# Optimization experiments

Hardware: AMD Instinct MI355X
Metric: run time of the kernel (lower is better)

The kernel has to match this reference:

```python
import jax, jax.numpy as jnp
import numpy as np
import math

B, S, E, D = 8, 2048, 1024, 1024  # batch, seq, emb_dim, encoder_emb_dim
LN_EPS = 1e-5
CLAMP = 1.0e9

def setup_inputs() -> dict:
    key = jax.random.key(0)
    ks = jax.random.split(key, 6)
    s = 1.0 / math.sqrt(E)
    return {
        "x": jax.random.normal(ks[0], (B, S, E), dtype=jnp.float32),
        "ln_w": jnp.ones((E,), jnp.float32),
        "ln_b": jnp.zeros((E,), jnp.float32),
        "wq": jax.random.normal(ks[1], (E, D), jnp.float32) * s,
        "bq": jnp.zeros((D,), jnp.float32),
        "wk": jax.random.normal(ks[2], (E, D), jnp.float32) * s,
        "bk": jnp.zeros((D,), jnp.float32),
        "wv": jax.random.normal(ks[3], (E, D), jnp.float32) * s,
        "bv": jnp.zeros((D,), jnp.float32),
        "w0": jax.random.normal(ks[4], (D, E), jnp.float32) * (1.0 / math.sqrt(D)),
        "b0": jnp.zeros((E,), jnp.float32),
    }

def reference(x, ln_w, ln_b, wq, bq, wk, bk, wv, bv, w0, b0):
    # LayerNorm over last dim (torch default eps=1e-5)
    mu = jnp.mean(x, axis=-1, keepdims=True)
    var = jnp.mean(jnp.square(x - mu), axis=-1, keepdims=True)
    xn = (x - mu) * jax.lax.rsqrt(var + LN_EPS) * ln_w + ln_b

    q = xn @ wq + bq  # [B,S,D]
    k = xn @ wk + bk
    v = xn @ wv + bv

    scale = math.sqrt(D) + 1e-9
    scores = jnp.einsum("bsd,btd->bst", q, k) / scale
    scores = jnp.clip(scores, -CLAMP, CLAMP)

    # masking=True, self_attending=True: mask = tril(ones, diagonal=-1)
    # i.e. positions t < s get -inf; diagonal stays unmasked (no NaN rows).
    mask = jnp.tril(jnp.ones((S, S), dtype=bool), k=-1)
    scores = jnp.where(mask, -jnp.inf, scores)

    a = jax.nn.softmax(scores, axis=-1)
    h = jnp.einsum("bst,btd->bsd", a, v)
    return h @ w0 + b0
```

## Files before the change

### kernel.cpp

```cpp
#include <hip/hip_runtime.h>
#include <cmath>

using u16 = unsigned short;
using u32 = unsigned int;
using bf16x8 = __attribute__((ext_vector_type(8))) __bf16;
using f32x4  = __attribute__((ext_vector_type(4))) float;

__device__ inline u16 f2bf(float f) {
  u32 u = __float_as_uint(f);
  u32 r = (u + 0x7fffu + ((u >> 16) & 1u)) >> 16;
  return (u16)r;
}

__global__ __launch_bounds__(256) void ln_kernel(
    const float* __restrict__ x, const float* __restrict__ w,
    const float* __restrict__ b, u16* __restrict__ xn) {
  int row = blockIdx.x;
  const float4* xr = (const float4*)(x + (size_t)row * 1024);
  float4 v = xr[threadIdx.x];
  float s  = v.x + v.y + v.z + v.w;
  float ss = v.x * v.x + v.y * v.y + v.z * v.z + v.w * v.w;
  int lane = threadIdx.x & 63, wave = threadIdx.x >> 6;
#pragma unroll
  for (int o = 32; o >= 1; o >>= 1) {
    s  += __shfl_xor(s, o, 64);
    ss += __shfl_xor(ss, o, 64);
  }
  __shared__ float rs[4], rq[4];
  if (lane == 0) { rs[wave] = s; rq[wave] = ss; }
  __syncthreads();
  s  = rs[0] + rs[1] + rs[2] + rs[3];
  ss = rq[0] + rq[1] + rq[2] + rq[3];
  float mean = s * (1.0f / 1024.0f);
  float var  = ss * (1.0f / 1024.0f) - mean * mean;
  float rstd = rsqrtf(var + 1e-5f);
  int c = threadIdx.x * 4;
  ushort4 ov;
  ov.x = f2bf((v.x - mean) * rstd * w[c + 0] + b[c + 0]);
  ov.y = f2bf((v.y - mean) * rstd * w[c + 1] + b[c + 1]);
  ov.z = f2bf((v.z - mean) * rstd * w[c + 2] + b[c + 2]);
  ov.w = f2bf((v.w - mean) * rstd * w[c + 3] + b[c + 3]);
  ((ushort4*)(xn + (size_t)row * 1024))[threadIdx.x] = ov;
}

__global__ __launch_bounds__(256) void transpose_w(
    const float* __restrict__ in, u16* __restrict__ out, int R, int C) {
  __shared__ float tile[32][33];
  int c0 = blockIdx.x * 32, r0 = blockIdx.y * 32;
  int tx = threadIdx.x, ty = threadIdx.y;
#pragma unroll
  for (int i = 0; i < 32; i += 8)
    tile[ty + i][tx] = in[(size_t)(r0 + ty + i) * C + c0 + tx];
  __syncthreads();
#pragma unroll
  for (int i = 0; i < 32; i += 8)
    out[(size_t)(c0 + ty + i) * R + r0 + tx] = f2bf(tile[tx][ty + i]);
}

__global__ void concat_bias(const float* __restrict__ bq, const float* __restrict__ bk,
                            const float* __restrict__ bv, float* __restrict__ o) {
  int i = blockIdx.x * 1024 + threadIdx.x;
  const float* src = (blockIdx.x == 0) ? bq : (blockIdx.x == 1) ? bk : bv;
  o[i] = src[threadIdx.x];
}

__global__ void rowinv_kernel(const float* __restrict__ sumP,
                              float* __restrict__ inv, int bA) {
  int r = blockIdx.x * 256 + threadIdx.x;
  int bz = bA + (r >> 11), s = r & 2047;
  float t = 0.f;
  for (int tj = s >> 8; tj < 8; ++tj)
    t += sumP[((size_t)bz * 8 + tj) * 2048 + s];
  inv[(size_t)bz * 2048 + s] = 1.0f / t;
}

template <int OUTF32, int MODE>
__global__ __launch_bounds__(512, 2) void gemm256(
    const u16* __restrict__ A, const u16* __restrict__ B, void* __restrict__ Cv,
    const float* __restrict__ bias, int K, int lda, int ldb, int ldc,
    float scale, long long sA, long long sB, long long sC) {
  int gx = gridDim.x;
  int wg = blockIdx.y * gx + blockIdx.x;
  {
    int nwg = gx * gridDim.y;
    if ((nwg & 7) == 0) {
      int q = nwg >> 3;
      wg = (wg & 7) * q + (wg >> 3);
    }
  }
  const int ti = wg / gx, tj = wg % gx, bz = blockIdx.z;
  if (MODE == 1 && tj < ti) return;

  const u16* Ab = A + (size_t)bz * (size_t)sA;
  const u16* Bb = B + (size_t)bz * (size_t)sB;

  __shared__ u16 As[2][256 * 64];
  __shared__ u16 Bs[2][256 * 64];

  const int tid = threadIdx.x;
  const int wave = tid >> 6, lane = tid & 63;
  const int wr = wave >> 2, wc = wave & 3;
  const int fr = lane & 15;
  const int kb16 = (lane >> 4) * 16;
  const int swz = (fr & 7) << 4;
  const int cs0 = kb16 ^ swz;
  const int cs1 = (64 + kb16) ^ swz;
  const int aRowOff = (wr * 128 + fr) * 128;
  const int bRowOff = (wc * 64 + fr) * 128;

  size_t gAo[2][2], gBo[2][2];
  u32 ldsA[2][2], ldsB[2][2];
#pragma unroll
  for (int h = 0; h < 2; ++h) {
#pragma unroll
    for (int l = 0; l < 2; ++l) {
      int i = l * 512 + tid;
      int rih = i >> 3, ch8 = i & 7;
      int rA = (rih & 63) + ((rih >> 6) << 7) + h * 64;
      int cbA = (ch8 << 4) ^ ((rA & 7) << 4);
      gAo[h][l] = (size_t)rA * lda + (cbA >> 1);
      ldsA[h][l] = (u32)(rA * 8 + ch8) * 16;
      int rB = (rih & 31) + ((rih >> 5) << 6) + h * 32;
      int cbB = (ch8 << 4) ^ ((rB & 7) << 4);
      gBo[h][l] = (size_t)rB * ldb + (cbB >> 1);
      ldsB[h][l] = (u32)(rB * 8 + ch8) * 16;
    }
  }
  const size_t aBase = (size_t)(ti * 256) * lda;
  const size_t bBase = (size_t)(tj * 256) * ldb;

  const int k0 = (MODE == 2) ? ti * 256 : 0;
  const int niter = (K - k0) / 128;

  f32x4 acc[8][4] = {};
  bf16x8 aF[4][2], bF[4][2];

#define GLL(gaddr, laddr)                                        \
  __builtin_amdgcn_global_load_lds(                              \
      (const __attribute__((address_space(1))) void*)(gaddr),    \
      (__attribute__((address_space(3))) void*)(laddr), 16, 0, 0)

#define STAGE_A(buf, h, t)                                                     \
  do {                                                                         \
    const size_t _kt = aBase + (size_t)(k0 + (t) * 64);                        \
    GLL(Ab + _kt + gAo[h][0], (char*)&As[buf][0] + ldsA[h][0]);                \
    GLL(Ab + _kt + gAo[h][1], (char*)&As[buf][0] + ldsA[h][1]);                \
  } while (0)
#define STAGE_B(buf, h, t)                                                     \
  do {                                                                         \
    const size_t _kt = bBase + (size_t)(k0 + (t) * 64);                        \
    GLL(Bb + _kt + gBo[h][0], (char*)&Bs[buf][0] + ldsB[h][0]);                \
    GLL(Bb + _kt + gBo[h][1], (char*)&Bs[buf][0] + ldsB[h][1]);                \
  } while (0)

#define DS_A(buf, qm)                                                \
  do {                                                               \
    const char* _pa = (const char*)&As[buf][0] + aRowOff + (qm)*8192;\
    _Pragma("unroll") for (int mm = 0; mm < 4; ++mm) {               \
      aF[mm][0] = *(const bf16x8*)(_pa + mm * 2048 + cs0);           \
      aF[mm][1] = *(const bf16x8*)(_pa + mm * 2048 + cs1);           \
    }                                                                \
  } while (0)
#define DS_B(buf, nh)                                                \
  do {                                                               \
    const char* _pb = (const char*)&Bs[buf][0] + bRowOff;            \
    _Pragma("unroll") for (int nn = 0; nn < 2; ++nn) {               \
      bF[(nh)*2 + nn][0] = *(const bf16x8*)(_pb + ((nh)*2 + nn) * 2048 + cs0); \
      bF[(nh)*2 + nn][1] = *(const bf16x8*)(_pb + ((nh)*2 + nn) * 2048 + cs1); \
    }                                                                \
  } while (0)

#define MMA(qm, nh)                                                          \
  do {                                                                       \
    _Pragma("unroll") for (int mm = 0; mm < 4; ++mm)                         \
    _Pragma("unroll") for (int nn = 0; nn < 2; ++nn) {                       \
      f32x4 _c = acc[(qm)*4 + mm][(nh)*2 + nn];                              \
      _c = __builtin_amdgcn_mfma_f32_16x16x32_bf16(aF[mm][0], bF[(nh)*2+nn][0], _c, 0, 0, 0); \
      _c = __builtin_amdgcn_mfma_f32_16x16x32_bf16(aF[mm][1], bF[(nh)*2+nn][1], _c, 0, 0, 0); \
      acc[(qm)*4 + mm][(nh)*2 + nn] = _c;                                    \
    }                                                                        \
  } while (0)

#define BAR __builtin_amdgcn_s_barrier()
#define LGKM0 asm volatile("s_waitcnt lgkmcnt(0)" ::: "memory")
#define VM6 asm volatile("s_waitcnt vmcnt(6)" ::: "memory")
#define VM0 asm volatile("s_waitcnt vmcnt(0)" ::: "memory")
#define PRIO1 __builtin_amdgcn_s_setprio(1)
#define PRIO0 __builtin_amdgcn_s_setprio(0)

  STAGE_B(0, 0, 0); STAGE_B(0, 1, 0); STAGE_A(0, 0, 0); STAGE_A(0, 1, 0);
  STAGE_B(1, 0, 1); STAGE_B(1, 1, 1); STAGE_A(1, 0, 1);
  VM6; BAR;

  for (int it = 0; it < niter; ++it) {
    const bool last = (it == niter - 1);
    const int t1g = 2 * it + 1, t2g = 2 * it + 2, t3g = 2 * it + 3;

    DS_A(0, 0); DS_B(0, 0);
    STAGE_A(1, 1, t1g);
    BAR; LGKM0; PRIO1; MMA(0, 0); PRIO0; BAR;
    DS_B(0, 1);
    if (!last) STAGE_B(0, 0, t2g);
    BAR; LGKM0; PRIO1; MMA(0, 1); PRIO0; BAR;
    DS_A(0, 1);
    if (!last) STAGE_B(0, 1, t2g);
    BAR; LGKM0; PRIO1; MMA(1, 0); PRIO0; BAR;
    if (!last) STAGE_A(0, 0, t2g);
    BAR; PRIO1; MMA(1, 1); PRIO0;
    if (last) { VM0; } else { VM6; }
    BAR;
    DS_A(1, 0); DS_B(1, 0);
    if (!last) STAGE_A(0, 1, t2g);
    BAR; LGKM0; PRIO1; MMA(0, 0); PRIO0; BAR;
    DS_B(1, 1);
    if (!last) STAGE_B(1, 0, t3g);
    BAR; LGKM0; PRIO1; MMA(0, 1); PRIO0; BAR;
    DS_A(1, 1);
    if (!last) STAGE_B(1, 1, t3g);
    BAR; LGKM0; PRIO1; MMA(1, 0); PRIO0; BAR;
    if (!last) STAGE_A(1, 0, t3g);
    BAR; PRIO1; MMA(1, 1); PRIO0;
    if (!last) VM6;
    BAR;
  }

  const int orow0 = ti * 256 + wr * 128 + ((lane >> 4) << 2);
  const int ocol0 = tj * 256 + wc * 64 + fr;
#pragma unroll
  for (int m = 0; m < 8; ++m) {
#pragma unroll
    for (int n = 0; n < 4; ++n) {
      const int col = ocol0 + n * 16;
      const float bv = bias ? bias[col] : 0.0f;
#pragma unroll
      for (int j = 0; j < 4; ++j) {
        const int row = orow0 + m * 16 + j;
        const float v = acc[m][n][j] * scale + bv;
        const size_t idx = (size_t)bz * (size_t)sC + (size_t)row * ldc + col;
        if (OUTF32) ((float*)Cv)[idx] = v;
        else        ((u16*)Cv)[idx]   = f2bf(v);
      }
    }
  }
#undef GLL
#undef STAGE_A
#undef STAGE_B
#undef DS_A
#undef DS_B
#undef MMA
#undef BAR
#undef LGKM0
#undef VM6
#undef VM0
#undef PRIO1
#undef PRIO0
}

template <int BM, int EPI, int LDA, int LDB, int LDC, int KK, int K0CT>
__device__ __forceinline__ void gemm_body(
    const u16* __restrict__ Ab, const u16* __restrict__ Bb,
    void* __restrict__ Cp, const float* __restrict__ bias,
    int rk0, float scale, size_t cbase, int ti, int tj,
    u16* __restrict__ AsP, u16* __restrict__ BsP,
    float* __restrict__ sumP, int diag, const float* __restrict__ invRow) {
  constexpr int WM = BM / 2;
  constexpr int MH = BM / 64;
  constexpr int FM = 2 * MH;
  constexpr int HR = BM / 4;
  constexpr int LA = BM / 128;

  const int k0 = (K0CT >= 0) ? K0CT : rk0;

  const int tid = threadIdx.x;
  const int wave = tid >> 6, lane = tid & 63;
  const int wr = wave >> 2, wc = wave & 3;
  const int fr = lane & 15;
  const int kb16 = (lane >> 4) * 16;
  const int swz = (fr & 7) << 4;
  const int cs0 = kb16 ^ swz;
  const int cs1 = (64 + kb16) ^ swz;
  const int aRowOff = (wr * WM + fr) * 128;
  const int bRowOff = (wc * 64 + fr) * 128;

  size_t gAo[2][LA], gBo[2][2];
  u32 ldsA[2][LA], ldsB[2][2];
#pragma unroll
  for (int h = 0; h < 2; ++h) {
#pragma unroll
    for (int l = 0; l < LA; ++l) {
      int i = l * 512 + tid;
      int rih = i >> 3, ch8 = i & 7;
      int rA = (rih % HR) + (rih / HR) * WM + h * HR;
      int cbA = (ch8 << 4) ^ ((rA & 7) << 4);
      gAo[h][l] = (size_t)rA * LDA + (cbA >> 1);
      ldsA[h][l] = (u32)(rA * 8 + ch8) * 16;
    }
#pragma unroll
    for (int l = 0; l < 2; ++l) {
      int i = l * 512 + tid;
      int rih = i >> 3, ch8 = i & 7;
      int rB = (rih & 31) + ((rih >> 5) << 6) + h * 32;
      int cbB = (ch8 << 4) ^ ((rB & 7) << 4);
      gBo[h][l] = (size_t)rB * LDB + (cbB >> 1);
      ldsB[h][l] = (u32)(rB * 8 + ch8) * 16;
    }
  }
  const size_t aBase = (size_t)(ti * BM) * LDA;
  const size_t bBase = (size_t)(tj * 256) * LDB;
  const int niter = (KK - k0) / 128;

  f32x4 acc[FM][4] = {};
  bf16x8 aF[MH][2], bF[4][2];

#define GLL(gaddr, laddr)                                        \
  __builtin_amdgcn_global_load_lds(                              \
      (const __attribute__((address_space(1))) void*)(gaddr),    \
      (__attribute__((address_space(3))) void*)(laddr), 16, 0, 0)

#define STAGE_A(buf, h, t)                                                   \
  do {                                                                       \
    const size_t _kt = aBase + (size_t)(k0 + (t) * 64);                      \
    _Pragma("unroll") for (int _l = 0; _l < LA; ++_l)                        \
        GLL(Ab + _kt + gAo[h][_l],                                           \
            (char*)(AsP + (buf) * (BM * 64)) + ldsA[h][_l]);                 \
  } while (0)
#define STAGE_B(buf, h, t)                                                   \
  do {                                                                       \
    const size_t _kt = bBase + (size_t)(k0 + (t) * 64);                      \
    _Pragma("unroll") for (int _l = 0; _l < 2; ++_l)                         \
        GLL(Bb + _kt + gBo[h][_l],                                           \
            (char*)(BsP + (buf) * (256 * 64)) + ldsB[h][_l]);                \
  } while (0)

#define DS_A(buf, qm)                                                        \
  do {                                                                       \
    const char* _pa =                                                        \
        (const char*)(AsP + (buf) * (BM * 64)) + aRowOff + (qm) * (MH * 2048); \
    _Pragma("unroll") for (int mm = 0; mm < MH; ++mm) {                      \
      aF[mm][0] = *(const bf16x8*)(_pa + mm * 2048 + cs0);                   \
      aF[mm][1] = *(const bf16x8*)(_pa + mm * 2048 + cs1);                   \
    }                                                                        \
  } while (0)
#define DS_B(buf, nh)                                                        \
  do {                                                                       \
    const char* _pb = (const char*)(BsP + (buf) * (256 * 64)) + bRowOff;     \
    _Pragma("unroll") for (int nn = 0; nn < 2; ++nn) {                       \
      bF[(nh)*2 + nn][0] = *(const bf16x8*)(_pb + ((nh)*2 + nn) * 2048 + cs0); \
      bF[(nh)*2 + nn][1] = *(const bf16x8*)(_pb + ((nh)*2 + nn) * 2048 + cs1); \
    }                                                                        \
  } while (0)

#define MMA(qm, nh)                                                          \
  do {                                                                       \
    _Pragma("unroll") for (int mm = 0; mm < MH; ++mm)                        \
    _Pragma("unroll") for (int nn = 0; nn < 2; ++nn) {                       \
      f32x4 _c = acc[(qm)*MH + mm][(nh)*2 + nn];                             \
      _c = __builtin_amdgcn_mfma_f32_16x16x32_bf16(aF[mm][0], bF[(nh)*2+nn][0], _c, 0, 0, 0); \
      _c = __builtin_amdgcn_mfma_f32_16x16x32_bf16(aF[mm][1], bF[(nh)*2+nn][1], _c, 0, 0, 0); \
      acc[(qm)*MH + mm][(nh)*2 + nn] = _c;                                   \
    }                                                                        \
  } while (0)

#define BAR __builtin_amdgcn_s_barrier()
#define LGKM0 asm volatile("s_waitcnt lgkmcnt(0)" ::: "memory")
#define VMN                                                                  \
  do {                                                                       \
    if constexpr (BM == 256)                                                 \
      asm volatile("s_waitcnt vmcnt(6)" ::: "memory");                       \
    else                                                                     \
      asm volatile("s_waitcnt vmcnt(5)" ::: "memory");                       \
  } while (0)
#define VM0 asm volatile("s_waitcnt vmcnt(0)" ::: "memory")
#define PRIO1 __builtin_amdgcn_s_setprio(1)
#define PRIO0 __builtin_amdgcn_s_setprio(0)

  STAGE_B(0, 0, 0); STAGE_B(0, 1, 0); STAGE_A(0, 0, 0); STAGE_A(0, 1, 0);
  STAGE_B(1, 0, 1); STAGE_B(1, 1, 1); STAGE_A(1, 0, 1);
  VMN; BAR;

#pragma unroll 1
  for (int it = 0; it < niter; ++it) {
    const bool last = (it == niter - 1);
    const int t1g = 2 * it + 1, t2g = 2 * it + 2, t3g = 2 * it + 3;

    DS_A(0, 0); DS_B(0, 0);
    STAGE_A(1, 1, t1g);
    BAR; LGKM0; PRIO1; MMA(0, 0); PRIO0; BAR;
    DS_B(0, 1);
    if (!last) STAGE_B(0, 0, t2g);
    BAR; LGKM0; PRIO1; MMA(0, 1); PRIO0; BAR;
    DS_A(0, 1);
    if (!last) STAGE_B(0, 1, t2g);
    BAR; LGKM0; PRIO1; MMA(1, 0); PRIO0; BAR;
    if (!last) STAGE_A(0, 0, t2g);
    BAR; PRIO1; MMA(1, 1); PRIO0;
    if (last) { VM0; } else { VMN; }
    BAR;
    DS_A(1, 0); DS_B(1, 0);
    if (!last) STAGE_A(0, 1, t2g);
    BAR; LGKM0; PRIO1; MMA(0, 0); PRIO0; BAR;
    DS_B(1, 1);
    if (!last) STAGE_B(1, 0, t3g);
    BAR; LGKM0; PRIO1; MMA(0, 1); PRIO0; BAR;
    DS_A(1, 1);
    if (!last) STAGE_B(1, 1, t3g);
    BAR; LGKM0; PRIO1; MMA(1, 0); PRIO0; BAR;
    if (!last) STAGE_A(1, 0, t3g);
    BAR; PRIO1; MMA(1, 1); PRIO0;
    if (!last) VMN;
    BAR;
  }

  const int orow0 = ti * BM + wr * WM + ((lane >> 4) << 2);
  const int ocol0 = tj * 256 + wc * 64 + fr;

  if constexpr (EPI == 1) {
    float* slds = (float*)AsP;
    const int rl0 = wr * WM + ((lane >> 4) << 2);
#pragma unroll
    for (int m = 0; m < FM; ++m) {
#pragma unroll
      for (int j = 0; j < 4; ++j) {
        const int rl = rl0 + m * 16 + j;
        const int row = ti * BM + rl;
        float rsum = 0.f;
#pragma unroll
        for (int n = 0; n < 4; ++n) {
          const int cl = wc * 64 + fr + n * 16;
          float v = acc[m][n][j] * scale;
          v = fminf(fmaxf(v, -1.0e9f), 1.0e9f);
          v = fminf(v, 60.0f);
          float e = __expf(v - 5.0f);
          if (diag && cl < rl) e = 0.f;
          rsum += e;
          ((u16*)Cp)[cbase + (size_t)row * LDC + ocol0 + n * 16] = f2bf(e);
        }
        rsum += __shfl_xor(rsum, 1, 64);
        rsum += __shfl_xor(rsum, 2, 64);
        rsum += __shfl_xor(rsum, 4, 64);
        rsum += __shfl_xor(rsum, 8, 64);
        if (fr == 0) slds[rl * 4 + wc] = rsum;
      }
    }
    __syncthreads();
    if (tid < 256) {
      float t = slds[tid * 4 + 0] + slds[tid * 4 + 1] +
                slds[tid * 4 + 2] + slds[tid * 4 + 3];
      sumP[ti * BM + tid] = t;
    }
  } else {
#pragma unroll
    for (int m = 0; m < FM; ++m) {
#pragma unroll
      for (int j = 0; j < 4; ++j) {
        const int row = orow0 + m * 16 + j;
        float mul = (EPI == 2) ? invRow[row] : 1.0f;
#pragma unroll
        for (int n = 0; n < 4; ++n) {
          const int col = ocol0 + n * 16;
          const float bv = bias ? bias[col] : 0.0f;
          const size_t idx = cbase + (size_t)row * LDC + col;
          if constexpr (EPI == 2) {
            ((float*)Cp)[idx] = acc[m][n][j] * mul + bv;
          } else {
            ((u16*)Cp)[idx] = f2bf(acc[m][n][j] + bv);
          }
        }
      }
    }
  }
#undef GLL
#undef STAGE_A
#undef STAGE_B
#undef DS_A
#undef DS_B
#undef MMA
#undef BAR
#undef LGKM0
#undef VMN
#undef VM0
#undef PRIO1
#undef PRIO0
}

__global__ __launch_bounds__(512, 2) void gemm_qkwt(
    const u16* __restrict__ QKVp, const u16* __restrict__ w0t,
    u16* __restrict__ Wt, u16* __restrict__ sc, float* __restrict__ sumP,
    int wtBlocks, int b0, int nb, float qk_scale) {
  __shared__ u16 As[2][256 * 64];
  __shared__ u16 Bs[2][256 * 64];
  const long long sQKV = 2048LL * 3072, sWt = 1024LL * 2048, sS = 2048LL * 2048;
  int x = blockIdx.x;
  if (x < wtBlocks) {
    int r = x & 7, o = x >> 3;
    int ti = o & 3, bztj = r + 8 * (o >> 2);
    int bz = bztj >> 3, tj = bztj & 7;
    gemm_body<256, 0, 1024, 3072, 2048, 1024, 0>(
        w0t, QKVp + (size_t)bz * sQKV + 2048, Wt, nullptr, 0, 1.0f,
        (size_t)bz * sWt, ti, tj, &As[0][0], &Bs[0][0], nullptr, 0, nullptr);
  } else {
    int q = x - wtBlocks;
    int bzl = q % nb, t36 = q / nb;
    int bz = b0 + bzl;
    int tj = 0, accm = 0;
    while (t36 >= accm + tj + 1) { accm += tj + 1; ++tj; }
    int tq = t36 - accm;
    const u16* Ab = QKVp + (size_t)bz * sQKV;
    gemm_body<256, 1, 3072, 3072, 2048, 1024, 0>(
        Ab, Ab + 1024, sc, nullptr, 0, qk_scale, (size_t)bzl * sS,
        tq, tj, &As[0][0], &Bs[0][0],
        sumP + ((size_t)bz * 8 + tj) * 2048, tq == tj, nullptr);
  }
}

__global__ __launch_bounds__(512, 2) void gemm_pv(
    const u16* __restrict__ sc, const u16* __restrict__ Wt,
    float* __restrict__ out, const float* __restrict__ b0v,
    const float* __restrict__ inv, int nb, int bA) {
  __shared__ u16 As[2][128 * 64];
  __shared__ u16 Bs[2][256 * 64];
  const long long sP = 2048LL * 2048, sWt = 1024LL * 2048, sH = 2048LL * 1024;
  int x = blockIdx.x;
  int bzl = x % nb;
  int rem = x / nb;
  int ti = rem >> 2, tj = rem & 3;
  int bz = bA + bzl;
  gemm_body<128, 2, 2048, 2048, 1024, 2048, -1>(
      sc + (size_t)bzl * sP, Wt + (size_t)bz * sWt, out, b0v, ti * 128, 1.0f,
      (size_t)bz * sH, ti, tj, &As[0][0], &Bs[0][0], nullptr, 0,
      inv + (size_t)bz * 2048);
}

extern "C" void kernel_launch(void* const* d_in, const int* in_sizes, int n_in,
                              void* d_out, int out_size, void* d_ws, size_t ws_size,
                              hipStream_t stream) {
  (void)in_sizes; (void)n_in; (void)out_size;
  const float* x   = (const float*)d_in[0];
  const float* lnw = (const float*)d_in[1];
  const float* lnb = (const float*)d_in[2];
  const float* wq  = (const float*)d_in[3];
  const float* bq  = (const float*)d_in[4];
  const float* wk  = (const float*)d_in[5];
  const float* bk  = (const float*)d_in[6];
  const float* wv  = (const float*)d_in[7];
  const float* bv  = (const float*)d_in[8];
  const float* w0  = (const float*)d_in[9];
  const float* b0  = (const float*)d_in[10];
  float* out = (float*)d_out;

  const size_t ROWS = 16384;
  char* ws = (char*)d_ws;
  size_t off = 0;
  auto alloc = [&](size_t bytes) -> void* {
    void* p = ws + off;
    off += (bytes + 255) & ~(size_t)255;
    return p;
  };
  u16*   xn    = (u16*)alloc(ROWS * 1024 * 2);
  u16*   wqkvt = (u16*)alloc((size_t)3072 * 1024 * 2);
  u16*   w0t   = (u16*)alloc((size_t)1024 * 1024 * 2);
  float* bqkv  = (float*)alloc(3072 * 4);
  float* sumP  = (float*)alloc((size_t)8 * 8 * 2048 * 4);
  float* inv   = (float*)alloc((size_t)8 * 2048 * 4);
  u16*   QKV   = (u16*)alloc(ROWS * 3072 * 2);
  u16*   Wt    = (u16*)alloc(ROWS * 1024 * 2);

  const size_t CHUNK1 = (size_t)2048 * 2048 * 2;
  size_t avail = (ws_size > off) ? ws_size - off : 0;
  int NBCH = (int)(avail / CHUNK1);
  if (NBCH > 8) NBCH = 8;
  if (NBCH < 1) NBCH = 1;
  u16* sc = (u16*)(ws + off);

  ln_kernel<<<dim3(16384), dim3(256), 0, stream>>>(x, lnw, lnb, xn);
  dim3 tb(32, 8);
  transpose_w<<<dim3(32, 32), tb, 0, stream>>>(wq, wqkvt, 1024, 1024);
  transpose_w<<<dim3(32, 32), tb, 0, stream>>>(wk, wqkvt + (size_t)1024 * 1024, 1024, 1024);
  transpose_w<<<dim3(32, 32), tb, 0, stream>>>(wv, wqkvt + (size_t)2048 * 1024, 1024, 1024);
  transpose_w<<<dim3(32, 32), tb, 0, stream>>>(w0, w0t, 1024, 1024);
  concat_bias<<<dim3(3), dim3(1024), 0, stream>>>(bq, bk, bv, bqkv);

  gemm256<0, 0><<<dim3(12, 64, 1), dim3(512), 0, stream>>>(
      xn, wqkvt, QKV, bqkv, 1024, 1024, 1024, 3072, 1.0f, 0, 0, 0);

  float qk_scale = (float)(1.0 / (std::sqrt(1024.0) + 1e-9));

  for (int bA = 0; bA < 8; bA += NBCH) {
    int nb = 8 - bA;
    if (nb > NBCH) nb = NBCH;
    int wtB = (bA == 0) ? 256 : 0;
    gemm_qkwt<<<dim3(wtB + nb * 36), dim3(512), 0, stream>>>(
        QKV, w0t, Wt, sc, sumP, wtB, bA, nb, qk_scale);
    rowinv_kernel<<<dim3(nb * 8), dim3(256), 0, stream>>>(sumP, inv, bA);
    gemm_pv<<<dim3(64 * nb), dim3(512), 0, stream>>>(
        sc, Wt, out, b0, inv, nb, bA);
  }
}
```

Measured before the change: 325.3 us.

## Fold row-inverse into PV GEMM, merge weight transposes, reorder QK/Wt blocks

The four weight transpose launches become one launch with a z-dimension. The separate rowinv kernel is removed: each PV GEMM workgroup now sums the partial softmax row sums and computes their reciprocals into LDS in its prologue. In the combined QK/Wt kernel, the QK score blocks are now dispatched first, and the Wt (w0ᵀ·V) blocks are split into 128-row tiles, twice as many blocks. Together these cut launch overhead, the global round-trip of the inverse array, and the tail imbalance. The cost is redundant row-sum work across column tiles of the PV GEMM.

```diff
diff --git a/kernel.cpp b/kernel.cpp
--- a/kernel.cpp
+++ b/kernel.cpp
@@ -43,18 +43,23 @@
   ((ushort4*)(xn + (size_t)row * 1024))[threadIdx.x] = ov;
 }
 
-__global__ __launch_bounds__(256) void transpose_w(
-    const float* __restrict__ in, u16* __restrict__ out, int R, int C) {
+__global__ __launch_bounds__(256) void transpose_w4(
+    const float* __restrict__ wq, const float* __restrict__ wk,
+    const float* __restrict__ wv, const float* __restrict__ w0,
+    u16* __restrict__ wqkvt, u16* __restrict__ w0t) {
+  int z = blockIdx.z;
+  const float* in = (z == 0) ? wq : (z == 1) ? wk : (z == 2) ? wv : w0;
+  u16* out = (z < 3) ? (wqkvt + (size_t)z * 1024 * 1024) : w0t;
   __shared__ float tile[32][33];
   int c0 = blockIdx.x * 32, r0 = blockIdx.y * 32;
   int tx = threadIdx.x, ty = threadIdx.y;
 #pragma unroll
   for (int i = 0; i < 32; i += 8)
-    tile[ty + i][tx] = in[(size_t)(r0 + ty + i) * C + c0 + tx];
+    tile[ty + i][tx] = in[(size_t)(r0 + ty + i) * 1024 + c0 + tx];
   __syncthreads();
 #pragma unroll
   for (int i = 0; i < 32; i += 8)
-    out[(size_t)(c0 + ty + i) * R + r0 + tx] = f2bf(tile[tx][ty + i]);
+    out[(size_t)(c0 + ty + i) * 1024 + r0 + tx] = f2bf(tile[tx][ty + i]);
 }
 
 __global__ void concat_bias(const float* __restrict__ bq, const float* __restrict__ bk,
@@ -62,16 +67,6 @@
   int i = blockIdx.x * 1024 + threadIdx.x;
   const float* src = (blockIdx.x == 0) ? bq : (blockIdx.x == 1) ? bk : bv;
   o[i] = src[threadIdx.x];
-}
-
-__global__ void rowinv_kernel(const float* __restrict__ sumP,
-                              float* __restrict__ inv, int bA) {
-  int r = blockIdx.x * 256 + threadIdx.x;
-  int bz = bA + (r >> 11), s = r & 2047;
-  float t = 0.f;
-  for (int tj = s >> 8; tj < 8; ++tj)
-    t += sumP[((size_t)bz * 8 + tj) * 2048 + s];
-  inv[(size_t)bz * 2048 + s] = 1.0f / t;
 }
 
 template <int OUTF32, int MODE>
@@ -262,7 +257,7 @@
     void* __restrict__ Cp, const float* __restrict__ bias,
     int rk0, float scale, size_t cbase, int ti, int tj,
     u16* __restrict__ AsP, u16* __restrict__ BsP,
-    float* __restrict__ sumP, int diag, const float* __restrict__ invRow) {
+    float* __restrict__ sumP, int diag) {
   constexpr int WM = BM / 2;
   constexpr int MH = BM / 64;
   constexpr int FM = 2 * MH;
@@ -281,6 +276,16 @@
   const int cs1 = (64 + kb16) ^ swz;
   const int aRowOff = (wr * WM + fr) * 128;
   const int bRowOff = (wc * 64 + fr) * 128;
+
+  __shared__ float invLds[(EPI == 2) ? BM : 1];
+  if constexpr (EPI == 2) {
+    if (tid < BM) {
+      int s = ti * BM + tid;
+      float a = 0.f;
+      for (int q2 = s >> 8; q2 < 8; ++q2) a += sumP[q2 * 2048 + s];
+      invLds[tid] = 1.0f / a;
+    }
+  }
 
   size_t gAo[2][LA], gBo[2][2];
   u32 ldsA[2][LA], ldsB[2][2];
@@ -411,17 +416,17 @@
     BAR;
   }
 
-  const int orow0 = ti * BM + wr * WM + ((lane >> 4) << 2);
+  const int orowL = wr * WM + ((lane >> 4) << 2);
+  const int orow0 = ti * BM + orowL;
   const int ocol0 = tj * 256 + wc * 64 + fr;
 
   if constexpr (EPI == 1) {
     float* slds = (float*)AsP;
-    const int rl0 = wr * WM + ((lane >> 4) << 2);
 #pragma unroll
     for (int m = 0; m < FM; ++m) {
 #pragma unroll
       for (int j = 0; j < 4; ++j) {
-        const int rl = rl0 + m * 16 + j;
+        const int rl = orowL + m * 16 + j;
         const int row = ti * BM + rl;
         float rsum = 0.f;
 #pragma unroll
@@ -443,7 +448,7 @@
       }
     }
     __syncthreads();
-    if (tid < 256) {
+    if (tid < BM) {
       float t = slds[tid * 4 + 0] + slds[tid * 4 + 1] +
                 slds[tid * 4 + 2] + slds[tid * 4 + 3];
       sumP[ti * BM + tid] = t;
@@ -454,7 +459,7 @@
 #pragma unroll
       for (int j = 0; j < 4; ++j) {
         const int row = orow0 + m * 16 + j;
-        float mul = (EPI == 2) ? invRow[row] : 1.0f;
+        float mul = (EPI == 2) ? invLds[orowL + m * 16 + j] : 1.0f;
 #pragma unroll
         for (int n = 0; n < 4; ++n) {
           const int col = ocol0 + n * 16;
@@ -486,21 +491,13 @@
 __global__ __launch_bounds__(512, 2) void gemm_qkwt(
     const u16* __restrict__ QKVp, const u16* __restrict__ w0t,
     u16* __restrict__ Wt, u16* __restrict__ sc, float* __restrict__ sumP,
-    int wtBlocks, int b0, int nb, float qk_scale) {
+    int qkBlocks, int b0, int nb, float qk_scale) {
   __shared__ u16 As[2][256 * 64];
   __shared__ u16 Bs[2][256 * 64];
   const long long sQKV = 2048LL * 3072, sWt = 1024LL * 2048, sS = 2048LL * 2048;
   int x = blockIdx.x;
-  if (x < wtBlocks) {
-    int r = x & 7, o = x >> 3;
-    int ti = o & 3, bztj = r + 8 * (o >> 2);
-    int bz = bztj >> 3, tj = bztj & 7;
-    gemm_body<256, 0, 1024, 3072, 2048, 1024, 0>(
-        w0t, QKVp + (size_t)bz * sQKV + 2048, Wt, nullptr, 0, 1.0f,
-        (size_t)bz * sWt, ti, tj, &As[0][0], &Bs[0][0], nullptr, 0, nullptr);
-  } else {
-    int q = x - wtBlocks;
-    int bzl = q % nb, t36 = q / nb;
+  if (x < qkBlocks) {
+    int bzl = x % nb, t36 = x / nb;
     int bz = b0 + bzl;
     int tj = 0, accm = 0;
     while (t36 >= accm + tj + 1) { accm += tj + 1; ++tj; }
@@ -509,14 +506,22 @@
     gemm_body<256, 1, 3072, 3072, 2048, 1024, 0>(
         Ab, Ab + 1024, sc, nullptr, 0, qk_scale, (size_t)bzl * sS,
         tq, tj, &As[0][0], &Bs[0][0],
-        sumP + ((size_t)bz * 8 + tj) * 2048, tq == tj, nullptr);
+        sumP + ((size_t)bz * 8 + tj) * 2048, tq == tj);
+  } else {
+    int x2 = x - qkBlocks;
+    int bz = x2 & 7;
+    int o = x2 >> 3;
+    int ti = o & 7, tj = o >> 3;
+    gemm_body<128, 0, 1024, 3072, 2048, 1024, 0>(
+        w0t, QKVp + (size_t)bz * sQKV + 2048, Wt, nullptr, 0, 1.0f,
+        (size_t)bz * sWt, ti, tj, &As[0][0], &Bs[0][0], nullptr, 0);
   }
 }
 
 __global__ __launch_bounds__(512, 2) void gemm_pv(
     const u16* __restrict__ sc, const u16* __restrict__ Wt,
     float* __restrict__ out, const float* __restrict__ b0v,
-    const float* __restrict__ inv, int nb, int bA) {
+    float* __restrict__ sumP, int nb, int bA) {
   __shared__ u16 As[2][128 * 64];
   __shared__ u16 Bs[2][256 * 64];
   const long long sP = 2048LL * 2048, sWt = 1024LL * 2048, sH = 2048LL * 1024;
@@ -527,8 +532,8 @@
   int bz = bA + bzl;
   gemm_body<128, 2, 2048, 2048, 1024, 2048, -1>(
       sc + (size_t)bzl * sP, Wt + (size_t)bz * sWt, out, b0v, ti * 128, 1.0f,
-      (size_t)bz * sH, ti, tj, &As[0][0], &Bs[0][0], nullptr, 0,
-      inv + (size_t)bz * 2048);
+      (size_t)bz * sH, ti, tj, &As[0][0], &Bs[0][0],
+      sumP + (size_t)bz * 8 * 2048, 0);
 }
 
 extern "C" void kernel_launch(void* const* d_in, const int* in_sizes, int n_in,
@@ -561,7 +566,6 @@
   u16*   w0t   = (u16*)alloc((size_t)1024 * 1024 * 2);
   float* bqkv  = (float*)alloc(3072 * 4);
   float* sumP  = (float*)alloc((size_t)8 * 8 * 2048 * 4);
-  float* inv   = (float*)alloc((size_t)8 * 2048 * 4);
   u16*   QKV   = (u16*)alloc(ROWS * 3072 * 2);
   u16*   Wt    = (u16*)alloc(ROWS * 1024 * 2);
 
@@ -573,11 +577,8 @@
   u16* sc = (u16*)(ws + off);
 
   ln_kernel<<<dim3(16384), dim3(256), 0, stream>>>(x, lnw, lnb, xn);
-  dim3 tb(32, 8);
-  transpose_w<<<dim3(32, 32), tb, 0, stream>>>(wq, wqkvt, 1024, 1024);
-  transpose_w<<<dim3(32, 32), tb, 0, stream>>>(wk, wqkvt + (size_t)1024 * 1024, 1024, 1024);
-  transpose_w<<<dim3(32, 32), tb, 0, stream>>>(wv, wqkvt + (size_t)2048 * 1024, 1024, 1024);
-  transpose_w<<<dim3(32, 32), tb, 0, stream>>>(w0, w0t, 1024, 1024);
+  transpose_w4<<<dim3(32, 32, 4), dim3(32, 8), 0, stream>>>(
+      wq, wk, wv, w0, wqkvt, w0t);
   concat_bias<<<dim3(3), dim3(1024), 0, stream>>>(bq, bk, bv, bqkv);
 
   gemm256<0, 0><<<dim3(12, 64, 1), dim3(512), 0, stream>>>(
@@ -588,11 +589,11 @@
   for (int bA = 0; bA < 8; bA += NBCH) {
     int nb = 8 - bA;
     if (nb > NBCH) nb = NBCH;
-    int wtB = (bA == 0) ? 256 : 0;
-    gemm_qkwt<<<dim3(wtB + nb * 36), dim3(512), 0, stream>>>(
-        QKV, w0t, Wt, sc, sumP, wtB, bA, nb, qk_scale);
-    rowinv_kernel<<<dim3(nb * 8), dim3(256), 0, stream>>>(sumP, inv, bA);
+    int qkB = nb * 36;
+    int wtB = (bA == 0) ? 512 : 0;
+    gemm_qkwt<<<dim3(qkB + wtB), dim3(512), 0, stream>>>(
+        QKV, w0t, Wt, sc, sumP, qkB, bA, nb, qk_scale);
     gemm_pv<<<dim3(64 * nb), dim3(512), 0, stream>>>(
-        sc, Wt, out, b0, inv, nb, bA);
-  }
-}
+        sc, Wt, out, b0, sumP, nb, bA);
+  }
+}
```

After: 304.7 us. 6.4% less time.
